# Kernel optimization log

Measured on AMD Instinct MI355X. Metric: run time of the kernel, lower is better.

Reference implementation:

```python
import jax, jax.numpy as jnp
import numpy as np
from jax import lax

HID = 128  # hidden_dim
K = 2      # kernel (must be 2 for the torch slice arithmetic to be shape-consistent)


def skew(x):
    # x: (B,C,H,W) -> (B,C,H,2W-1), row r shifted right by r
    B, C, H, W = x.shape
    rows = jnp.arange(H)[:, None]
    cols = jnp.arange(W)[None, :] + rows
    y = jnp.zeros((B, C, H, 2 * W - 1), x.dtype)
    return y.at[:, :, rows, cols].set(x)


def unskew(x):
    B, C, H, Wp = x.shape
    W = (Wp + 1) // 2
    rows = jnp.arange(H)[:, None]
    cols = jnp.arange(W)[None, :] + rows
    return x[:, :, rows, cols]


def setup_inputs() -> dict:
    key = jax.random.key(0)
    k1, k2, k3 = jax.random.split(key, 3)
    Cin = 128
    x = jax.random.normal(k1, (8, Cin, 64, 64), jnp.float32)
    w_is = jax.random.normal(k2, (4 * HID, Cin), jnp.float32) * 0.05   # 1x1 conv weight
    b_is = jnp.zeros((4 * HID,), jnp.float32)
    w_ss = jax.random.normal(k3, (4 * HID, HID, K, 1), jnp.float32) * 0.05  # (k,1) conv weight
    b_ss = jnp.zeros((4 * HID,), jnp.float32)
    return {"x": x, "w_is": w_is, "b_is": b_is, "w_ss": w_ss, "b_ss": b_ss}


def reference(x, w_is, b_is, w_ss, b_ss):
    B, Cin, H, W = x.shape
    hid, k = HID, K
    xs = skew(x)  # (B,Cin,H,2W-1)
    # input-to-state: 1x1 conv (mask B on 1x1 kernel == plain 1x1 conv)
    z_is = jnp.einsum('bchw,oc->bohw', xs, w_is) + b_is[None, :, None, None]
    steps = z_is.transpose(3, 0, 1, 2)  # (2W-1, B, 4hid, H)

    h0 = jnp.zeros((B, hid, H), x.dtype)
    c0 = jnp.zeros((B, hid, H), x.dtype)

    def step(carry, z_t):
        h, c = carry  # (B,hid,H)
        # state-to-state (k,1) conv along H, padding k//2, then drop last k-1 rows
        hs = lax.conv_general_dilated(h[..., None], w_ss, (1, 1),
                                      [(k // 2, k // 2), (0, 0)],
                                      dimension_numbers=('NCHW', 'OIHW', 'NCHW'))
        hs = hs[:, :, :-(k - 1), 0] + b_ss[None, :, None]  # (B,4hid,H)
        z = z_t + hs
        i = jax.nn.sigmoid(z[:, :hid])
        f = jax.nn.sigmoid(z[:, hid:2 * hid])
        o = jax.nn.sigmoid(z[:, 2 * hid:3 * hid])
        g = jnp.tanh(z[:, 3 * hid:])
        c = f * c + i * g
        h = o * jnp.tanh(c)
        return (h, c), h

    _, hs_all = lax.scan(step, (h0, c0), steps)  # (2W-1,B,hid,H)
    out = hs_all.transpose(1, 2, 3, 0)  # (B,hid,H,2W-1)
    return unskew(out)  # (B,hid,H,W)
```

## Files before the change

### kernel.cpp

```cpp
#include <hip/hip_runtime.h>
#include <hip/hip_fp16.h>
#include <math.h>


#define HID 128
#define BB 8
#define HH 64
#define WW 64
#define TT 127

typedef _Float16 v8h __attribute__((ext_vector_type(8)));
typedef float v4f __attribute__((ext_vector_type(4)));

#define SENT64 0x7E007E007E007E00ULL

__device__ __forceinline__ float fsig(float x) {
  x = __builtin_fmaxf(__builtin_fminf(x, 30.f), -30.f);
  float e = __builtin_amdgcn_exp2f(x * -1.44269504f);
  return __builtin_amdgcn_rcpf(1.f + e);
}
__device__ __forceinline__ float ftanh_(float x) {
  x = __builtin_fmaxf(__builtin_fminf(x, 15.f), -15.f);
  float e = __builtin_amdgcn_exp2f(x * 2.88539009f);
  return (e - 1.f) * __builtin_amdgcn_rcpf(e + 1.f);
}

__global__ __launch_bounds__(256) void prep_all(
    const float* __restrict__ w_ss, const float* __restrict__ w_is,
    _Float16* __restrict__ wp, _Float16* __restrict__ wisa,
    unsigned long long* __restrict__ hx) {
  int idx = blockIdx.x * 256 + threadIdx.x;
  if (idx < 131072) {
    int j = idx & 7;
    int L = (idx >> 3) & 63;
    int kt = (idx >> 9) & 7;
    int mt = idx >> 12;
    int O = mt * 16 + (L & 15);
    int k = kt * 32 + ((L >> 4) & 3) * 8 + j;
    float v = (k < 128) ? w_ss[(size_t)O * 256 + k * 2]
                        : w_ss[(size_t)O * 256 + (k - 128) * 2 + 1];
    wp[idx] = (_Float16)v;
  } else if (idx < 196608) {
    int i2 = idx - 131072;
    int j = i2 & 7;
    int L = (i2 >> 3) & 63;
    int kt = (i2 >> 9) & 3;
    int mt = i2 >> 11;
    int O = mt * 16 + (L & 15);
    int k = kt * 32 + ((L >> 4) & 3) * 8 + j;
    wisa[i2] = (_Float16)w_is[(size_t)O * 128 + k];
  } else if (idx < 196608 + TT * 8 * 4 * 64) {
    hx[idx - 196608] = SENT64;
  }
}

__global__ __launch_bounds__(256) void zpre_mfma(const float* __restrict__ x,
                                                 const _Float16* __restrict__ wisa,
                                                 __half* __restrict__ zph) {
  const int b = blockIdx.x >> 6;
  const int r = blockIdx.x & 63;
  const int tid = threadIdx.x;
  const int wv = tid >> 6;
  const int L = tid & 63;
  const int quad = L >> 4;
  const int l15 = L & 15;

  __shared__ _Float16 xt[64][136];

  {
    int c = tid >> 1;
    int wh = (tid & 1) * 32;
    const float4* xs =
        (const float4*)&x[(((size_t)b * 128 + c) * HH + r) * WW + wh];
#pragma unroll
    for (int i = 0; i < 8; i++) {
      float4 v = xs[i];
      xt[wh + 4 * i + 0][c] = (_Float16)v.x;
      xt[wh + 4 * i + 1][c] = (_Float16)v.y;
      xt[wh + 4 * i + 2][c] = (_Float16)v.z;
      xt[wh + 4 * i + 3][c] = (_Float16)v.w;
    }
  }
  __syncthreads();

  const int wcol = wv * 16 + l15;
  v8h bf[4];
#pragma unroll
  for (int kt = 0; kt < 4; kt++)
    bf[kt] = *(const v8h*)&xt[wcol][kt * 32 + quad * 8];

  const size_t pos = ((size_t)b * HH + r) * WW + wcol;
  const v8h* wa8 = (const v8h*)wisa;

#pragma unroll 4
  for (int mt = 0; mt < 32; mt++) {
    v4f acc = (v4f){0.f, 0.f, 0.f, 0.f};
#pragma unroll
    for (int kt = 0; kt < 4; kt++) {
      v8h af = wa8[((size_t)mt * 4 + kt) * 64 + L];
      acc = __builtin_amdgcn_mfma_f32_16x16x32_f16(af, bf[kt], acc, 0, 0, 0);
    }
    __half2 lo = __floats2half2_rn(acc[0], acc[1]);
    __half2 hi = __floats2half2_rn(acc[2], acc[3]);
    uint2 pk;
    pk.x = *(unsigned*)&lo;
    pk.y = *(unsigned*)&hi;
    *(uint2*)&zph[pos * 512 + ((mt & 7) * 4 + quad) * 16 + (mt >> 3) * 4] = pk;
  }
}

#define HROW 136

__global__ __launch_bounds__(512, 1) void lstm_mfma(
    const __half* __restrict__ zph, const _Float16* __restrict__ wp,
    const float* __restrict__ b_is, const float* __restrict__ b_ss,
    unsigned long long* __restrict__ hx,
    float* __restrict__ out) {
  const int blk = blockIdx.x;
  const int rgr = blk >> 2;
  const int bg = blk & 3;
  const int R0 = rgr * 8;
  const int tid = threadIdx.x;
  const int wv = tid >> 6;
  const int L = tid & 63;
  const int quad = L >> 4;
  const int l15 = L & 15;
  const int rl = l15 >> 1;
  const int bl = l15 & 1;
  const int b = bg * 2 + bl;
  const int r = R0 + rl;
  const int uq0 = 16 * wv + quad * 4;
  const int zoff = (4 * wv + quad) * 16;

  __shared__ _Float16 h_lds[2][9 * 2 * HROW];
  for (int i = tid; i < (2 * 9 * 2 * HROW) / 2; i += 512)
    ((unsigned*)h_lds)[i] = 0u;

  v8h wfrag[4][8];
  {
    const v8h* wp8 = (const v8h*)wp;
#pragma unroll
    for (int g = 0; g < 4; g++)
#pragma unroll
      for (int kt = 0; kt < 8; kt++)
        wfrag[g][kt] = wp8[((size_t)((8 * g + wv) * 8 + kt)) * 64 + L];
  }

  float bsum[4][4];
#pragma unroll
  for (int g = 0; g < 4; g++)
#pragma unroll
    for (int rg2 = 0; rg2 < 4; rg2++) {
      int O = g * 128 + uq0 + rg2;
      bsum[g][rg2] = b_is[O] + b_ss[O];
    }

  float c[4] = {0.f, 0.f, 0.f, 0.f};
  float4 outb[4];
#pragma unroll
  for (int i = 0; i < 4; i++) outb[i] = make_float4(0.f, 0.f, 0.f, 0.f);

  const int ebl = L >> 5;
  const int eu = (L & 31) * 4;
  const int exp_idx = bl * 32 + 4 * wv + quad;

  const bool is_cons = (wv == 0) && (rgr > 0);

  union ZU {
    uint4 q[2];
    __half h[16];
  } zu;
  zu.q[0] = (uint4){0u, 0u, 0u, 0u};
  zu.q[1] = (uint4){0u, 0u, 0u, 0u};
  if (r == 0) {
    const uint4* p = (const uint4*)(zph + ((size_t)b * HH * WW) * 512 + zoff);
    zu.q[0] = p[0];
    zu.q[1] = p[1];
  }

  unsigned long long pend = 0ull;
  if (is_cons) {
    pend = __hip_atomic_load(&hx[(((size_t)0 * 8 + (rgr - 1)) * 4 + bg) * 64 + L],
                             __ATOMIC_RELAXED, __HIP_MEMORY_SCOPE_AGENT);
  }

  __syncthreads();

  for (int t = 0; t < TT; t++) {
    const int rb = t & 1;
    const int wb = rb ^ 1;

    unsigned long long newp = 0ull;
    if (is_cons && (t + 1) < TT) {
      newp = __hip_atomic_load(
          &hx[(((size_t)(t + 1) * 8 + (rgr - 1)) * 4 + bg) * 64 + L],
          __ATOMIC_RELAXED, __HIP_MEMORY_SCOPE_AGENT);
    }

    v4f acc[4];
#pragma unroll
    for (int g = 0; g < 4; g++) acc[g] = (v4f){0.f, 0.f, 0.f, 0.f};
#pragma unroll
    for (int kt = 0; kt < 8; kt++) {
      const int slot = (kt < 4) ? rl : (rl + 1);
      v8h bf = *(const v8h*)&h_lds[rb][(slot * 2 + bl) * HROW +
                                       (kt & 3) * 32 + quad * 8];
#pragma unroll
      for (int g = 0; g < 4; g++)
        acc[g] = __builtin_amdgcn_mfma_f32_16x16x32_f16(wfrag[g][kt], bf,
                                                        acc[g], 0, 0, 0);
    }

    const int w = t - r;
    const bool inband = (w >= 0) && (w < WW);
    float hv[4];
#pragma unroll
    for (int rg2 = 0; rg2 < 4; rg2++) {
      float z0 = acc[0][rg2] + bsum[0][rg2] + __half2float(zu.h[0 * 4 + rg2]);
      float z1 = acc[1][rg2] + bsum[1][rg2] + __half2float(zu.h[1 * 4 + rg2]);
      float z2 = acc[2][rg2] + bsum[2][rg2] + __half2float(zu.h[2 * 4 + rg2]);
      float z3 = acc[3][rg2] + bsum[3][rg2] + __half2float(zu.h[3 * 4 + rg2]);
      float iv = fsig(z0);
      float fv = fsig(z1);
      float ov = fsig(z2);
      float gv = ftanh_(z3);
      c[rg2] = fv * c[rg2] + iv * gv;
      hv[rg2] = ov * ftanh_(c[rg2]);
    }

    {
      __half2 lo = __floats2half2_rn(hv[0], hv[1]);
      __half2 hi = __floats2half2_rn(hv[2], hv[3]);
      uint2 pk;
      pk.x = *(unsigned*)&lo;
      pk.y = *(unsigned*)&hi;
      *(uint2*)&h_lds[wb][((rl + 1) * 2 + bl) * HROW + uq0] = pk;
    }

    if (rgr < 7 && l15 >= 14) {
      __half2 lo = __floats2half2_rn(hv[0], hv[1]);
      __half2 hi = __floats2half2_rn(hv[2], hv[3]);
      unsigned long long pk =
          ((unsigned long long)*(unsigned*)&hi << 32) | *(unsigned*)&lo;
      __hip_atomic_store(&hx[(((size_t)t * 8 + rgr) * 4 + bg) * 64 + exp_idx],
                         pk, __ATOMIC_RELAXED, __HIP_MEMORY_SCOPE_AGENT);
    }

#pragma unroll
    for (int rg2 = 0; rg2 < 4; rg2++) {
      outb[rg2].x = outb[rg2].y;
      outb[rg2].y = outb[rg2].z;
      outb[rg2].z = outb[rg2].w;
      outb[rg2].w = hv[rg2];
    }
    if (inband && (w & 3) == 3) {
      float* op_ = out + (((size_t)b * HID + uq0) * HH + r) * WW + (w - 3);
#pragma unroll
      for (int rg2 = 0; rg2 < 4; rg2++) {
        *(float4*)(op_ + (size_t)rg2 * (HH * WW)) = outb[rg2];
      }
    }

    {
      const int wn = t + 1 - r;
      if (wn >= 0 && wn < WW) {
        const uint4* p =
            (const uint4*)(zph + (((size_t)b * HH + r) * WW + wn) * 512 + zoff);
        zu.q[0] = p[0];
        zu.q[1] = p[1];
      } else {
        zu.q[0] = (uint4){0u, 0u, 0u, 0u};
        zu.q[1] = (uint4){0u, 0u, 0u, 0u};
      }
    }

    if (is_cons) {
      const unsigned long long* addr =
          &hx[(((size_t)t * 8 + (rgr - 1)) * 4 + bg) * 64 + L];
      while (__ballot(pend == SENT64) != 0ull) {
        __builtin_amdgcn_s_sleep(1);
        pend = __hip_atomic_load(addr, __ATOMIC_RELAXED,
                                 __HIP_MEMORY_SCOPE_AGENT);
      }
      *(unsigned long long*)&h_lds[wb][(0 * 2 + ebl) * HROW + eu] = pend;
      pend = newp;
    }

    __syncthreads();
  }
}

__global__ __launch_bounds__(256) void transpose_x(const float* __restrict__ x,
                                                   float* __restrict__ xT) {
  int b = blockIdx.x >> 6;
  int r = blockIdx.x & 63;
  __shared__ float tile[32][65];
  for (int cc = 0; cc < 4; cc++) {
    int cl = threadIdx.x >> 6;
    int w = threadIdx.x & 63;
#pragma unroll
    for (int k = 0; k < 8; k++) {
      int c_loc = k * 4 + cl;
      int c = cc * 32 + c_loc;
      tile[c_loc][w] = x[(((size_t)b * 128 + c) * HH + r) * WW + w];
    }
    __syncthreads();
    int cs = threadIdx.x & 31;
    int wp = threadIdx.x >> 5;
#pragma unroll
    for (int k = 0; k < 8; k++) {
      int w2 = wp * 8 + k;
      xT[(((size_t)b * HH + r) * WW + w2) * 128 + cc * 32 + cs] = tile[cs][w2];
    }
    __syncthreads();
  }
}

__global__ __launch_bounds__(256) void step_kernel(
    const float* __restrict__ x, const float* __restrict__ xT, int use_xT,
    const float* __restrict__ w_is, const float* __restrict__ b_is,
    const float* __restrict__ w_ss, const float* __restrict__ b_ss,
    const float* __restrict__ h_prev, float* __restrict__ h_next,
    float* __restrict__ c_state, float* __restrict__ out, int t) {
  const int rg = blockIdx.x;
  const int q = blockIdx.y;
  const int r0 = rg * 2;
  const int tid = threadIdx.x;
  const int o_loc = tid & 63;
  const int k4 = tid >> 6;
  const int g_ = o_loc >> 4;
  const int u_ = o_loc & 15;
  const int O = g_ * 128 + q * 16 + u_;
  const int i0 = k4 * 32;

  __shared__ __align__(16) float h_in[3][BB][HID];
  __shared__ float zred[16][4][65];

  for (int idx = tid; idx < 3 * BB * HID; idx += 256) {
    int row_sel = idx >> 10;
    int rem = idx & 1023;
    int b = rem >> 7;
    int u = rem & 127;
    int rr = r0 - 1 + row_sel;
    h_in[row_sel][b][u] = (rr >= 0) ? h_prev[((size_t)b * HH + rr) * HID + u] : 0.0f;
  }

  float wr0[32], wr1[32], wz[32];
  {
    const float4* wss4 = (const float4*)(w_ss + ((size_t)O * 128 + i0) * 2);
#pragma unroll
    for (int j = 0; j < 16; j++) {
      float4 v = wss4[j];
      wr0[2 * j] = v.x;
      wr1[2 * j] = v.y;
      wr0[2 * j + 1] = v.z;
      wr1[2 * j + 1] = v.w;
    }
    const float4* wis4 = (const float4*)(w_is + (size_t)O * 128 + i0);
#pragma unroll
    for (int j = 0; j < 8; j++) {
      float4 v = wis4[j];
      wz[4 * j] = v.x;
      wz[4 * j + 1] = v.y;
      wz[4 * j + 2] = v.z;
      wz[4 * j + 3] = v.w;
    }
  }

  __syncthreads();

  float acc[2][BB];
#pragma unroll
  for (int rl = 0; rl < 2; rl++)
#pragma unroll
    for (int b = 0; b < BB; b++) acc[rl][b] = 0.0f;

#pragma unroll
  for (int jb = 0; jb < 8; jb++) {
    int ib = i0 + jb * 4;
#pragma unroll
    for (int b = 0; b < BB; b++) {
      const float4 hm4 = *(const float4*)&h_in[0][b][ib];
      const float4 hc4 = *(const float4*)&h_in[1][b][ib];
      const float4 hp4 = *(const float4*)&h_in[2][b][ib];
      const float* hm = (const float*)&hm4;
      const float* hc = (const float*)&hc4;
      const float* hq = (const float*)&hp4;
#pragma unroll
      for (int jj = 0; jj < 4; jj++) {
        float w0v = wr0[jb * 4 + jj];
        float w1v = wr1[jb * 4 + jj];
        acc[0][b] += w0v * hm[jj] + w1v * hc[jj];
        acc[1][b] += w0v * hc[jj] + w1v * hq[jj];
      }
    }
  }

#pragma unroll
  for (int rl = 0; rl < 2; rl++) {
    int rr = r0 + rl;
    int wcol = t - rr;
    if (wcol >= 0 && wcol < WW) {
      if (use_xT) {
        for (int b = 0; b < BB; b++) {
          const float4* xp =
              (const float4*)(xT + (((size_t)b * HH + rr) * WW + wcol) * 128 + i0);
#pragma unroll
          for (int j = 0; j < 8; j++) {
            float4 v = xp[j];
            acc[rl][b] += wz[4 * j] * v.x + wz[4 * j + 1] * v.y +
                          wz[4 * j + 2] * v.z + wz[4 * j + 3] * v.w;
          }
        }
      } else {
        for (int b = 0; b < BB; b++) {
          const float* xb = x + (((size_t)b * 128 + i0) * HH + rr) * WW + wcol;
#pragma unroll
          for (int j = 0; j < 32; j++) {
            acc[rl][b] += wz[j] * xb[(size_t)j * HH * WW];
          }
        }
      }
    }
  }

#pragma unroll
  for (int rl = 0; rl < 2; rl++)
#pragma unroll
    for (int b = 0; b < BB; b++) zred[rl * 8 + b][k4][o_loc] = acc[rl][b];
  __syncthreads();

  {
    int u = tid >> 4;
    int cell = tid & 15;
    int rl = cell >> 3;
    int b = cell & 7;
    int rr = r0 + rl;
    float z[4];
#pragma unroll
    for (int gg = 0; gg < 4; gg++) {
      int ol = gg * 16 + u;
      float s = zred[cell][0][ol] + zred[cell][1][ol] + zred[cell][2][ol] +
                zred[cell][3][ol];
      int Og = gg * 128 + q * 16 + u;
      z[gg] = s + b_is[Og] + b_ss[Og];
    }
    float iv = 1.0f / (1.0f + expf(-z[0]));
    float fv = 1.0f / (1.0f + expf(-z[1]));
    float ov = 1.0f / (1.0f + expf(-z[2]));
    float gv = tanhf(z[3]);
    int U = q * 16 + u;
    size_t sidx = ((size_t)b * HH + rr) * HID + U;
    float cv = c_state[sidx];
    float cn = fv * cv + iv * gv;
    c_state[sidx] = cn;
    float hn = ov * tanhf(cn);
    h_next[sidx] = hn;
    int wcol = t - rr;
    if (wcol >= 0 && wcol < WW) {
      out[(((size_t)b * HID + U) * HH + rr) * WW + wcol] = hn;
    }
  }
}

extern "C" void kernel_launch(void* const* d_in, const int* in_sizes, int n_in,
                              void* d_out, int out_size, void* d_ws,
                              size_t ws_size, hipStream_t stream) {
  const float* x = (const float*)d_in[0];
  const float* w_is = (const float*)d_in[1];
  const float* b_is = (const float*)d_in[2];
  const float* w_ss = (const float*)d_in[3];
  const float* b_ss = (const float*)d_in[4];
  float* outp = (float*)d_out;

  const size_t zph_bytes = (size_t)BB * HH * WW * 512 * 2;
  const size_t wp_bytes = (size_t)512 * 256 * 2;
  const size_t wisa_bytes = (size_t)512 * 128 * 2;
  const size_t hx_bytes = (size_t)TT * 8 * 4 * 64 * 8;
  const size_t need = zph_bytes + wp_bytes + wisa_bytes + hx_bytes;

  char* ws = (char*)d_ws;
  if (ws_size >= need) {
    __half* zph = (__half*)ws;
    _Float16* wpp = (_Float16*)(ws + zph_bytes);
    _Float16* wisa = (_Float16*)(ws + zph_bytes + wp_bytes);
    unsigned long long* hx =
        (unsigned long long*)(ws + zph_bytes + wp_bytes + wisa_bytes);

    prep_all<<<dim3(1784), 256, 0, stream>>>(w_ss, w_is, wpp, wisa, hx);
    zpre_mfma<<<dim3(BB * HH), 256, 0, stream>>>(x, wisa, zph);
    lstm_mfma<<<dim3(32), 512, 0, stream>>>(zph, wpp, b_is, b_ss, hx, outp);
  } else {
    const size_t xT_elems = (size_t)BB * HH * WW * 128;
    const size_t st_elems = (size_t)BB * HH * HID;
    const size_t need_xT = (xT_elems + 3 * st_elems) * sizeof(float);
    float* wsf = (float*)d_ws;
    float* xT = nullptr;
    float* st;
    int use_xT = 0;
    if (ws_size >= need_xT) {
      use_xT = 1;
      xT = wsf;
      st = wsf + xT_elems;
    } else {
      st = wsf;
    }
    float* h0 = st;
    float* h1 = st + st_elems;
    float* cb = st + 2 * st_elems;
    hipMemsetAsync(st, 0, 3 * st_elems * sizeof(float), stream);
    if (use_xT) transpose_x<<<dim3(BB * HH), 256, 0, stream>>>(x, xT);
    for (int t = 0; t < TT; t++) {
      float* hp = (t & 1) ? h1 : h0;
      float* hn = (t & 1) ? h0 : h1;
      step_kernel<<<dim3(32, 8), 256, 0, stream>>>(x, xT, use_xT, w_is, b_is,
                                                   w_ss, b_ss, hp, hn, cb, outp,
                                                   t);
    }
  }
}
```

Baseline: 347.3 us.

## Fuse input projection into LSTM kernel with sentinel-flagged producer/consumer overlap

Merges the zpre input-projection GEMM into the recurrent LSTM kernel. Blocks 0-31 run the recurrence while the extra 256 blocks compute the z pre-activations concurrently. zph is pre-filled with NaN sentinels in prep_all, and the recurrent blocks spin on atomic loads until the values they need have been written. This hides the projection behind the serial scan and removes one launch, but adds a sentinel fill of the whole zph buffer and polling traffic. It also depends on the recurrent blocks being co-resident with the producer blocks, or the spin-waits can deadlock.

```diff
diff --git a/kernel.cpp b/kernel.cpp
--- a/kernel.cpp
+++ b/kernel.cpp
@@ -28,7 +28,7 @@
 __global__ __launch_bounds__(256) void prep_all(
     const float* __restrict__ w_ss, const float* __restrict__ w_is,
     _Float16* __restrict__ wp, _Float16* __restrict__ wisa,
-    unsigned long long* __restrict__ hx) {
+    unsigned long long* __restrict__ hx, __half* __restrict__ zph) {
   int idx = blockIdx.x * 256 + threadIdx.x;
   if (idx < 131072) {
     int j = idx & 7;
@@ -49,78 +49,89 @@
     int O = mt * 16 + (L & 15);
     int k = kt * 32 + ((L >> 4) & 3) * 8 + j;
     wisa[i2] = (_Float16)w_is[(size_t)O * 128 + k];
-  } else if (idx < 196608 + TT * 8 * 4 * 64) {
+  } else if (idx < 456704) {
     hx[idx - 196608] = SENT64;
-  }
-}
-
-__global__ __launch_bounds__(256) void zpre_mfma(const float* __restrict__ x,
-                                                 const _Float16* __restrict__ wisa,
-                                                 __half* __restrict__ zph) {
-  const int b = blockIdx.x >> 6;
-  const int r = blockIdx.x & 63;
-  const int tid = threadIdx.x;
-  const int wv = tid >> 6;
-  const int L = tid & 63;
-  const int quad = L >> 4;
-  const int l15 = L & 15;
-
-  __shared__ _Float16 xt[64][136];
-
-  {
-    int c = tid >> 1;
-    int wh = (tid & 1) * 32;
-    const float4* xs =
-        (const float4*)&x[(((size_t)b * 128 + c) * HH + r) * WW + wh];
-#pragma unroll
-    for (int i = 0; i < 8; i++) {
-      float4 v = xs[i];
-      xt[wh + 4 * i + 0][c] = (_Float16)v.x;
-      xt[wh + 4 * i + 1][c] = (_Float16)v.y;
-      xt[wh + 4 * i + 2][c] = (_Float16)v.z;
-      xt[wh + 4 * i + 3][c] = (_Float16)v.w;
-    }
-  }
-  __syncthreads();
-
-  const int wcol = wv * 16 + l15;
-  v8h bf[4];
-#pragma unroll
-  for (int kt = 0; kt < 4; kt++)
-    bf[kt] = *(const v8h*)&xt[wcol][kt * 32 + quad * 8];
-
-  const size_t pos = ((size_t)b * HH + r) * WW + wcol;
-  const v8h* wa8 = (const v8h*)wisa;
-
-#pragma unroll 4
-  for (int mt = 0; mt < 32; mt++) {
-    v4f acc = (v4f){0.f, 0.f, 0.f, 0.f};
-#pragma unroll
-    for (int kt = 0; kt < 4; kt++) {
-      v8h af = wa8[((size_t)mt * 4 + kt) * 64 + L];
-      acc = __builtin_amdgcn_mfma_f32_16x16x32_f16(af, bf[kt], acc, 0, 0, 0);
-    }
-    __half2 lo = __floats2half2_rn(acc[0], acc[1]);
-    __half2 hi = __floats2half2_rn(acc[2], acc[3]);
-    uint2 pk;
-    pk.x = *(unsigned*)&lo;
-    pk.y = *(unsigned*)&hi;
-    *(uint2*)&zph[pos * 512 + ((mt & 7) * 4 + quad) * 16 + (mt >> 3) * 4] = pk;
+  } else if (idx < 456704 + 2097152) {
+    uint4 s;
+    s.x = 0x7E007E00u;
+    s.y = 0x7E007E00u;
+    s.z = 0x7E007E00u;
+    s.w = 0x7E007E00u;
+    ((uint4*)zph)[idx - 456704] = s;
   }
 }
 
 #define HROW 136
 
-__global__ __launch_bounds__(512, 1) void lstm_mfma(
-    const __half* __restrict__ zph, const _Float16* __restrict__ wp,
+__global__ __launch_bounds__(512, 2) void lstm_fused(
+    const float* __restrict__ x, const _Float16* __restrict__ wisa,
+    __half* __restrict__ zph, const _Float16* __restrict__ wp,
     const float* __restrict__ b_is, const float* __restrict__ b_ss,
     unsigned long long* __restrict__ hx,
     float* __restrict__ out) {
   const int blk = blockIdx.x;
+  const int tid = threadIdx.x;
+  __shared__ __align__(16) _Float16 smem[2 * 64 * HROW];
+
+  if (blk >= 32) {
+    const int half = tid >> 8;
+    const int t2 = tid & 255;
+    const int posi = (blk - 32) * 2 + half;
+    const int b = posi >> 6;
+    const int r = posi & 63;
+    _Float16* xt = smem + half * (64 * HROW);
+
+    {
+      int c = t2 >> 1;
+      int wh = (t2 & 1) * 32;
+      const float4* xs =
+          (const float4*)&x[(((size_t)b * 128 + c) * HH + r) * WW + wh];
+#pragma unroll
+      for (int i = 0; i < 8; i++) {
+        float4 v = xs[i];
+        xt[(wh + 4 * i + 0) * HROW + c] = (_Float16)v.x;
+        xt[(wh + 4 * i + 1) * HROW + c] = (_Float16)v.y;
+        xt[(wh + 4 * i + 2) * HROW + c] = (_Float16)v.z;
+        xt[(wh + 4 * i + 3) * HROW + c] = (_Float16)v.w;
+      }
+    }
+    __syncthreads();
+
+    const int L = t2 & 63;
+    const int wv2 = t2 >> 6;
+    const int quad = L >> 4;
+    const int l15 = L & 15;
+    const int wcol = wv2 * 16 + l15;
+    v8h bf[4];
+#pragma unroll
+    for (int kt = 0; kt < 4; kt++)
+      bf[kt] = *(const v8h*)&xt[wcol * HROW + kt * 32 + quad * 8];
+
+    const size_t pos = ((size_t)b * HH + r) * WW + wcol;
+    unsigned long long* zp64 = (unsigned long long*)zph;
+    const v8h* wa8 = (const v8h*)wisa;
+
+#pragma unroll 4
+    for (int mt = 0; mt < 32; mt++) {
+      v4f acc = (v4f){0.f, 0.f, 0.f, 0.f};
+#pragma unroll
+      for (int kt = 0; kt < 4; kt++) {
+        v8h af = wa8[((size_t)mt * 4 + kt) * 64 + L];
+        acc = __builtin_amdgcn_mfma_f32_16x16x32_f16(af, bf[kt], acc, 0, 0, 0);
+      }
+      __half2 lo = __floats2half2_rn(acc[0], acc[1]);
+      __half2 hi = __floats2half2_rn(acc[2], acc[3]);
+      unsigned long long pk =
+          ((unsigned long long)*(unsigned*)&hi << 32) | *(unsigned*)&lo;
+      __hip_atomic_store(&zp64[pos * 128 + ((mt & 7) * 4 + quad) * 4 + (mt >> 3)],
+                         pk, __ATOMIC_RELAXED, __HIP_MEMORY_SCOPE_AGENT);
+    }
+    return;
+  }
+
   const int rgr = blk >> 2;
   const int bg = blk & 3;
   const int R0 = rgr * 8;
-  const int tid = threadIdx.x;
   const int wv = tid >> 6;
   const int L = tid & 63;
   const int quad = L >> 4;
@@ -130,11 +141,11 @@
   const int b = bg * 2 + bl;
   const int r = R0 + rl;
   const int uq0 = 16 * wv + quad * 4;
-  const int zoff = (4 * wv + quad) * 16;
-
-  __shared__ _Float16 h_lds[2][9 * 2 * HROW];
+
+  _Float16* h_lds0 = smem;
+  _Float16* h_lds1 = smem + 9 * 2 * HROW;
   for (int i = tid; i < (2 * 9 * 2 * HROW) / 2; i += 512)
-    ((unsigned*)h_lds)[i] = 0u;
+    ((unsigned*)smem)[i] = 0u;
 
   v8h wfrag[4][8];
   {
@@ -163,19 +174,22 @@
   const int ebl = L >> 5;
   const int eu = (L & 31) * 4;
   const int exp_idx = bl * 32 + 4 * wv + quad;
-
   const bool is_cons = (wv == 0) && (rgr > 0);
+  const unsigned long long* zph64 = (const unsigned long long*)zph;
+  const int zgi = (4 * wv + quad) * 4;
 
   union ZU {
-    uint4 q[2];
+    unsigned long long q[4];
     __half h[16];
   } zu;
-  zu.q[0] = (uint4){0u, 0u, 0u, 0u};
-  zu.q[1] = (uint4){0u, 0u, 0u, 0u};
+#pragma unroll
+  for (int g = 0; g < 4; g++) zu.q[g] = 0ull;
   if (r == 0) {
-    const uint4* p = (const uint4*)(zph + ((size_t)b * HH * WW) * 512 + zoff);
-    zu.q[0] = p[0];
-    zu.q[1] = p[1];
+    size_t zi = (size_t)b * HH * WW * 128 + zgi;
+#pragma unroll
+    for (int g = 0; g < 4; g++)
+      zu.q[g] = __hip_atomic_load(&zph64[zi + g], __ATOMIC_RELAXED,
+                                  __HIP_MEMORY_SCOPE_AGENT);
   }
 
   unsigned long long pend = 0ull;
@@ -187,8 +201,8 @@
   __syncthreads();
 
   for (int t = 0; t < TT; t++) {
-    const int rb = t & 1;
-    const int wb = rb ^ 1;
+    _Float16* rbuf = (t & 1) ? h_lds1 : h_lds0;
+    _Float16* wbuf = (t & 1) ? h_lds0 : h_lds1;
 
     unsigned long long newp = 0ull;
     if (is_cons && (t + 1) < TT) {
@@ -203,16 +217,34 @@
 #pragma unroll
     for (int kt = 0; kt < 8; kt++) {
       const int slot = (kt < 4) ? rl : (rl + 1);
-      v8h bf = *(const v8h*)&h_lds[rb][(slot * 2 + bl) * HROW +
-                                       (kt & 3) * 32 + quad * 8];
+      v8h bfr = *(const v8h*)&rbuf[(slot * 2 + bl) * HROW +
+                                   (kt & 3) * 32 + quad * 8];
 #pragma unroll
       for (int g = 0; g < 4; g++)
-        acc[g] = __builtin_amdgcn_mfma_f32_16x16x32_f16(wfrag[g][kt], bf,
+        acc[g] = __builtin_amdgcn_mfma_f32_16x16x32_f16(wfrag[g][kt], bfr,
                                                         acc[g], 0, 0, 0);
     }
 
     const int w = t - r;
     const bool inband = (w >= 0) && (w < WW);
+
+    {
+      bool bad = inband && ((zu.q[0] == SENT64) || (zu.q[1] == SENT64) ||
+                            (zu.q[2] == SENT64) || (zu.q[3] == SENT64));
+      while (__ballot(bad) != 0ull) {
+        __builtin_amdgcn_s_sleep(1);
+        if (bad) {
+          size_t zi = (((size_t)b * HH + r) * WW + w) * 128 + zgi;
+#pragma unroll
+          for (int g = 0; g < 4; g++)
+            zu.q[g] = __hip_atomic_load(&zph64[zi + g], __ATOMIC_RELAXED,
+                                        __HIP_MEMORY_SCOPE_AGENT);
+          bad = (zu.q[0] == SENT64) || (zu.q[1] == SENT64) ||
+                (zu.q[2] == SENT64) || (zu.q[3] == SENT64);
+        }
+      }
+    }
+
     float hv[4];
 #pragma unroll
     for (int rg2 = 0; rg2 < 4; rg2++) {
@@ -234,7 +266,7 @@
       uint2 pk;
       pk.x = *(unsigned*)&lo;
       pk.y = *(unsigned*)&hi;
-      *(uint2*)&h_lds[wb][((rl + 1) * 2 + bl) * HROW + uq0] = pk;
+      *(uint2*)&wbuf[((rl + 1) * 2 + bl) * HROW + uq0] = pk;
     }
 
     if (rgr < 7 && l15 >= 14) {
@@ -264,13 +296,14 @@
     {
       const int wn = t + 1 - r;
       if (wn >= 0 && wn < WW) {
-        const uint4* p =
-            (const uint4*)(zph + (((size_t)b * HH + r) * WW + wn) * 512 + zoff);
-        zu.q[0] = p[0];
-        zu.q[1] = p[1];
+        size_t zi = (((size_t)b * HH + r) * WW + wn) * 128 + zgi;
+#pragma unroll
+        for (int g = 0; g < 4; g++)
+          zu.q[g] = __hip_atomic_load(&zph64[zi + g], __ATOMIC_RELAXED,
+                                      __HIP_MEMORY_SCOPE_AGENT);
       } else {
-        zu.q[0] = (uint4){0u, 0u, 0u, 0u};
-        zu.q[1] = (uint4){0u, 0u, 0u, 0u};
+#pragma unroll
+        for (int g = 0; g < 4; g++) zu.q[g] = 0ull;
       }
     }
 
@@ -282,7 +315,7 @@
         pend = __hip_atomic_load(addr, __ATOMIC_RELAXED,
                                  __HIP_MEMORY_SCOPE_AGENT);
       }
-      *(unsigned long long*)&h_lds[wb][(0 * 2 + ebl) * HROW + eu] = pend;
+      *(unsigned long long*)&wbuf[(0 * 2 + ebl) * HROW + eu] = pend;
       pend = newp;
     }
 
@@ -487,9 +520,9 @@
     unsigned long long* hx =
         (unsigned long long*)(ws + zph_bytes + wp_bytes + wisa_bytes);
 
-    prep_all<<<dim3(1784), 256, 0, stream>>>(w_ss, w_is, wpp, wisa, hx);
-    zpre_mfma<<<dim3(BB * HH), 256, 0, stream>>>(x, wisa, zph);
-    lstm_mfma<<<dim3(32), 512, 0, stream>>>(zph, wpp, b_is, b_ss, hx, outp);
+    prep_all<<<dim3(9976), 256, 0, stream>>>(w_ss, w_is, wpp, wisa, hx, zph);
+    lstm_fused<<<dim3(288), 512, 0, stream>>>(x, wisa, zph, wpp, b_is, b_ss,
+                                              hx, outp);
   } else {
     const size_t xT_elems = (size_t)BB * HH * WW * 128;
     const size_t st_elems = (size_t)BB * HH * HID;
```

Measured after the change: 465.5 us. 1.34x slower.
